# Optimization experiments

Measured on AMD Instinct MI355X. Metric: run time of the kernel, lower is better.

The kernel has to match this reference:

```python
import jax, jax.numpy as jnp
import numpy as np

PARENTS = [-1, 0, 0, 0, 1, 2, 3, 4, 5, 6, 7, 8, 9, 9, 9, 12, 13, 14, 16, 17, 18, 19, 20, 21]
J = len(PARENTS)  # 24
B = 524288
EPS = 1e-8


def _bfs_order(parents):
    children = {i: [] for i in range(len(parents))}
    for j, p in enumerate(parents):
        if p >= 0:
            children[p].append(j)
    order = [0]
    i = 0
    while i < len(order):
        order.extend(children[order[i]])
        i += 1
    return order

BFS_ORDER = _bfs_order(PARENTS)


def setup_inputs() -> dict:
    key = jax.random.key(0)
    k1, k2, k3, k4, k5 = jax.random.split(key, 5)
    root_orientation_quat = jax.random.normal(k1, (B, 4), dtype=jnp.float32)
    root_position = jax.random.normal(k2, (B, 3), dtype=jnp.float32)
    local_joint_rotations_quat = jax.random.normal(k3, (B, J, 4), dtype=jnp.float32)
    bone_lengths = jax.random.uniform(k4, (B, J), dtype=jnp.float32, minval=0.05, maxval=0.5)
    rest_directions = jax.random.normal(k5, (J, 3), dtype=jnp.float32)
    rest_directions = rest_directions / (jnp.linalg.norm(rest_directions, axis=-1, keepdims=True) + EPS)
    return {
        'root_orientation_quat': root_orientation_quat,
        'root_position': root_position,
        'local_joint_rotations_quat': local_joint_rotations_quat,
        'bone_lengths': bone_lengths,
        'rest_directions': rest_directions,
    }


def _quat_mul(p, c):
    # Hamilton product, (w, x, y, z) layout; p, c: [B, 4]
    pw, px, py, pz = p[:, 0], p[:, 1], p[:, 2], p[:, 3]
    cw, cx, cy, cz = c[:, 0], c[:, 1], c[:, 2], c[:, 3]
    return jnp.stack([
        pw * cw - px * cx - py * cy - pz * cz,
        pw * cx + px * cw + py * cz - pz * cy,
        pw * cy - px * cz + py * cw + pz * cx,
        pw * cz + px * cy - py * cx + pz * cw,
    ], axis=-1)


def reference(root_orientation_quat, root_position, local_joint_rotations_quat, bone_lengths, rest_directions):
    root_q = root_orientation_quat / (jnp.linalg.norm(root_orientation_quat, axis=-1, keepdims=True) + EPS)
    local_q = local_joint_rotations_quat / (jnp.linalg.norm(local_joint_rotations_quat, axis=-1, keepdims=True) + EPS)

    glob_q = [None] * J
    glob_p = [None] * J
    glob_q[0] = root_q
    glob_p[0] = root_position

    for j in BFS_ORDER:
        p = PARENTS[j]
        if p == -1:
            continue
        pq = glob_q[p]              # [B, 4] parent global orientation
        glob_q[j] = _quat_mul(pq, local_q[:, j, :])
        # rotate unit rest direction by parent global quaternion:
        # v' = v + qw * t + qvec x t, where t = 2 * (qvec x v)
        qvec = pq[:, 1:]            # [B, 3]
        qw = pq[:, 0:1]             # [B, 1]
        d = rest_directions[j][None, :]  # [1, 3] broadcast over batch
        t = 2.0 * jnp.cross(qvec, jnp.broadcast_to(d, qvec.shape), axis=1)
        rotated = d + qw * t + jnp.cross(qvec, t, axis=1)
        glob_p[j] = glob_p[p] + rotated * bone_lengths[:, j:j + 1]

    return jnp.stack(glob_p, axis=1)  # [B, J, 3]
```

## Files before the change

kernel.cpp:

```cpp
#include <hip/hip_runtime.h>
#include <math.h>


#define NB 524288
#define NJ 24
#define BLOCK 256
#define LSTR 257

namespace {
constexpr int PAR[NJ] = {-1,0,0,0,1,2,3,4,5,6,7,8,9,9,9,12,13,14,16,17,18,19,20,21};
}

__global__ __launch_bounds__(BLOCK)
void ForwardKinematics_51342039056994_kernel(
    const float* __restrict__ root_q,
    const float* __restrict__ root_p,
    const float* __restrict__ loc_q,
    const float* __restrict__ bones,
    const float* __restrict__ rest_d,
    float* __restrict__ out)
{
    __shared__ float lds[24 * LSTR];

    const int tid = threadIdx.x;
    const int blockBase = blockIdx.x * BLOCK;
    const int b = blockBase + tid;

    float gqw[NJ], gqx[NJ], gqy[NJ], gqz[NJ];
    float gpx[NJ], gpy[NJ], gpz[NJ];

    float4 rq = ((const float4*)root_q)[b];
    float rpx = root_p[b*3+0], rpy = root_p[b*3+1], rpz = root_p[b*3+2];
    {
        float inv = 1.0f / (sqrtf(rq.x*rq.x + rq.y*rq.y + rq.z*rq.z + rq.w*rq.w) + 1e-8f);
        gqw[0] = rq.x * inv; gqx[0] = rq.y * inv; gqy[0] = rq.z * inv; gqz[0] = rq.w * inv;
    }
    gpx[0] = rpx; gpy[0] = rpy; gpz[0] = rpz;

    const float4* lsrc = (const float4*)loc_q + (size_t)b * NJ;
    const float4* bsrc = (const float4*)(bones + (size_t)b * NJ);
    float4* outv = (float4*)out;

    float4 lq[8];
    #pragma unroll
    for (int i = 0; i < 8; ++i) lq[i] = lsrc[i];
    float4 bq0 = bsrc[0], bq1 = bsrc[1];

    #define DO_JOINT(j, lqv, L)                                                 \
    {                                                                           \
        const int p_ = PAR[(j)];                                                \
        float lw = (lqv).x, lx = (lqv).y, ly = (lqv).z, lz = (lqv).w;           \
        float invn = 1.0f / (sqrtf(lw*lw + lx*lx + ly*ly + lz*lz) + 1e-8f);     \
        lw *= invn; lx *= invn; ly *= invn; lz *= invn;                         \
        const float pw  = gqw[p_], px_ = gqx[p_], py_ = gqy[p_], pz_ = gqz[p_]; \
        gqw[(j)] = pw*lw - px_*lx - py_*ly - pz_*lz;                            \
        gqx[(j)] = pw*lx + px_*lw + py_*lz - pz_*ly;                            \
        gqy[(j)] = pw*ly - px_*lz + py_*lw + pz_*lx;                            \
        gqz[(j)] = pw*lz + px_*ly - py_*lx + pz_*lw;                            \
        const float dx = rest_d[3*(j)+0];                                       \
        const float dy = rest_d[3*(j)+1];                                       \
        const float dz = rest_d[3*(j)+2];                                       \
        float tx = 2.0f*(py_*dz - pz_*dy);                                      \
        float ty = 2.0f*(pz_*dx - px_*dz);                                      \
        float tz = 2.0f*(px_*dy - py_*dx);                                      \
        float rx = dx + pw*tx + (py_*tz - pz_*ty);                              \
        float ry = dy + pw*ty + (pz_*tx - px_*tz);                              \
        float rz = dz + pw*tz + (px_*ty - py_*tx);                              \
        gpx[(j)] = gpx[p_] + rx*(L);                                            \
        gpy[(j)] = gpy[p_] + ry*(L);                                            \
        gpz[(j)] = gpz[p_] + rz*(L);                                            \
    }

    #pragma unroll
    for (int c = 0; c < 3; ++c) {
        float4 nlq[8]; float4 nb0, nb1;
        if (c < 2) {
            #pragma unroll
            for (int i = 0; i < 8; ++i) nlq[i] = lsrc[8*(c+1) + i];
            nb0 = bsrc[2*(c+1) + 0];
            nb1 = bsrc[2*(c+1) + 1];
        }

        float bl[8] = {bq0.x, bq0.y, bq0.z, bq0.w, bq1.x, bq1.y, bq1.z, bq1.w};

        #pragma unroll
        for (int jj = 0; jj < 8; ++jj) {
            const int j = 8*c + jj;
            if (j > 0) DO_JOINT(j, lq[jj], bl[jj]);
            lds[(jj*3 + 0) * LSTR + tid] = gpx[j];
            lds[(jj*3 + 1) * LSTR + tid] = gpy[j];
            lds[(jj*3 + 2) * LSTR + tid] = gpz[j];
        }

        __syncthreads();

        #pragma unroll
        for (int m = 0; m < 6; ++m) {
            int g = m * BLOCK + tid;
            int t = g / 6;
            int k = g - 6 * t;
            float4 v;
            v.x = lds[(4*k + 0) * LSTR + t];
            v.y = lds[(4*k + 1) * LSTR + t];
            v.z = lds[(4*k + 2) * LSTR + t];
            v.w = lds[(4*k + 3) * LSTR + t];
            outv[(size_t)(blockBase + t) * 18 + c * 6 + k] = v;
        }

        __syncthreads();

        if (c < 2) {
            #pragma unroll
            for (int i = 0; i < 8; ++i) lq[i] = nlq[i];
            bq0 = nb0; bq1 = nb1;
        }
    }
    #undef DO_JOINT
}

extern "C" void kernel_launch(void* const* d_in, const int* in_sizes, int n_in,
                              void* d_out, int out_size, void* d_ws, size_t ws_size,
                              hipStream_t stream) {
    (void)in_sizes; (void)n_in; (void)out_size; (void)d_ws; (void)ws_size;
    const float* root_q = (const float*)d_in[0];
    const float* root_p = (const float*)d_in[1];
    const float* loc_q  = (const float*)d_in[2];
    const float* bones  = (const float*)d_in[3];
    const float* rest_d = (const float*)d_in[4];
    float* out = (float*)d_out;

    dim3 grid(NB / BLOCK);
    dim3 block(BLOCK);
    ForwardKinematics_51342039056994_kernel<<<grid, block, 0, stream>>>(
        root_q, root_p, loc_q, bones, rest_d, out);
}
```

Measured before the change: 407.4 us.

## Use single-wave blocks and one end-of-kernel LDS transpose without barriers

New measurement: 366.2 us. 10.1% less time.

```diff
diff --git a/kernel.cpp b/kernel.cpp
--- a/kernel.cpp
+++ b/kernel.cpp
@@ -4,8 +4,9 @@
 
 #define NB 524288
 #define NJ 24
-#define BLOCK 256
-#define LSTR 257
+#define BLOCK 64
+#define ROWS 72
+#define LSTR 65
 
 namespace {
 constexpr int PAR[NJ] = {-1,0,0,0,1,2,3,4,5,6,7,8,9,9,9,12,13,14,16,17,18,19,20,21};
@@ -20,11 +21,11 @@
     const float* __restrict__ rest_d,
     float* __restrict__ out)
 {
-    __shared__ float lds[24 * LSTR];
+    __shared__ float wlds[ROWS * LSTR];
 
-    const int tid = threadIdx.x;
-    const int blockBase = blockIdx.x * BLOCK;
-    const int b = blockBase + tid;
+    const int lane = threadIdx.x;
+    const int waveBase = blockIdx.x * BLOCK;
+    const int b = waveBase + lane;
 
     float gqw[NJ], gqx[NJ], gqy[NJ], gqz[NJ];
     float gpx[NJ], gpy[NJ], gpz[NJ];
@@ -36,15 +37,12 @@
         gqw[0] = rq.x * inv; gqx[0] = rq.y * inv; gqy[0] = rq.z * inv; gqz[0] = rq.w * inv;
     }
     gpx[0] = rpx; gpy[0] = rpy; gpz[0] = rpz;
+    wlds[0 * LSTR + lane] = rpx;
+    wlds[1 * LSTR + lane] = rpy;
+    wlds[2 * LSTR + lane] = rpz;
 
     const float4* lsrc = (const float4*)loc_q + (size_t)b * NJ;
     const float4* bsrc = (const float4*)(bones + (size_t)b * NJ);
-    float4* outv = (float4*)out;
-
-    float4 lq[8];
-    #pragma unroll
-    for (int i = 0; i < 8; ++i) lq[i] = lsrc[i];
-    float4 bq0 = bsrc[0], bq1 = bsrc[1];
 
     #define DO_JOINT(j, lqv, L)                                                 \
     {                                                                           \
@@ -69,7 +67,15 @@
         gpx[(j)] = gpx[p_] + rx*(L);                                            \
         gpy[(j)] = gpy[p_] + ry*(L);                                            \
         gpz[(j)] = gpz[p_] + rz*(L);                                            \
+        wlds[(3*(j) + 0) * LSTR + lane] = gpx[(j)];                             \
+        wlds[(3*(j) + 1) * LSTR + lane] = gpy[(j)];                             \
+        wlds[(3*(j) + 2) * LSTR + lane] = gpz[(j)];                             \
     }
+
+    float4 lq[8];
+    #pragma unroll
+    for (int i = 0; i < 8; ++i) lq[i] = lsrc[i];
+    float4 bq0 = bsrc[0], bq1 = bsrc[1];
 
     #pragma unroll
     for (int c = 0; c < 3; ++c) {
@@ -87,27 +93,7 @@
         for (int jj = 0; jj < 8; ++jj) {
             const int j = 8*c + jj;
             if (j > 0) DO_JOINT(j, lq[jj], bl[jj]);
-            lds[(jj*3 + 0) * LSTR + tid] = gpx[j];
-            lds[(jj*3 + 1) * LSTR + tid] = gpy[j];
-            lds[(jj*3 + 2) * LSTR + tid] = gpz[j];
         }
-
-        __syncthreads();
-
-        #pragma unroll
-        for (int m = 0; m < 6; ++m) {
-            int g = m * BLOCK + tid;
-            int t = g / 6;
-            int k = g - 6 * t;
-            float4 v;
-            v.x = lds[(4*k + 0) * LSTR + t];
-            v.y = lds[(4*k + 1) * LSTR + t];
-            v.z = lds[(4*k + 2) * LSTR + t];
-            v.w = lds[(4*k + 3) * LSTR + t];
-            outv[(size_t)(blockBase + t) * 18 + c * 6 + k] = v;
-        }
-
-        __syncthreads();
 
         if (c < 2) {
             #pragma unroll
@@ -116,6 +102,20 @@
         }
     }
     #undef DO_JOINT
+
+    float4* outv = (float4*)out + (size_t)waveBase * 18;
+    #pragma unroll
+    for (int m = 0; m < 18; ++m) {
+        int g = m * 64 + lane;
+        int t = g / 18;
+        int k = g - 18 * t;
+        float4 v;
+        v.x = wlds[(4*k + 0) * LSTR + t];
+        v.y = wlds[(4*k + 1) * LSTR + t];
+        v.z = wlds[(4*k + 2) * LSTR + t];
+        v.w = wlds[(4*k + 3) * LSTR + t];
+        outv[g] = v;
+    }
 }
 
 extern "C" void kernel_launch(void* const* d_in, const int* in_sizes, int n_in,
```
